# Kernel optimization log

Hardware: AMD Instinct MI355X
Metric: run time of the kernel (lower is better)

## Reference

```python
import jax, jax.numpy as jnp
import numpy as np

EPS = 1e-5
N, K, C = 32768, 27, 128


def setup_inputs() -> dict:
    key = jax.random.key(0)
    k1, k2, k3, k4 = jax.random.split(key, 4)
    feats = jax.random.normal(k1, (N, C), dtype=jnp.float32)
    # Precomputed kernel-offset neighbor map (MinkowskiEngine kernel map),
    # one input index per (point, kernel offset).
    neighbors = jax.random.randint(k2, (N, K), 0, N, dtype=jnp.int32)
    scale = 1.0 / np.sqrt(K * C)  # fan-in init like sparse conv
    W1 = jax.random.normal(k3, (K, C, C), dtype=jnp.float32) * scale
    W2 = jax.random.normal(k4, (K, C, C), dtype=jnp.float32) * scale
    g1 = jnp.ones((C,), jnp.float32)
    b1 = jnp.zeros((C,), jnp.float32)
    g2 = jnp.ones((C,), jnp.float32)
    b2 = jnp.zeros((C,), jnp.float32)
    return {"feats": feats, "neighbors": neighbors, "W1": W1, "g1": g1,
            "b1": b1, "W2": W2, "g2": g2, "b2": b2}


def _sparse_conv(f, nbr, W):
    # gather-GEMM-scatter: gather neighbor features per kernel offset,
    # contract with that offset's weight, sum over offsets.
    gathered = f[nbr]                      # [N, K, C]
    return jnp.einsum('nkc,kcd->nd', gathered, W)  # [N, C]


def _batch_norm(x, gamma, beta):
    mu = jnp.mean(x, axis=0)
    var = jnp.mean(jnp.square(x - mu), axis=0)
    return (x - mu) * jax.lax.rsqrt(var + EPS) * gamma + beta


def reference(feats, neighbors, W1, g1, b1, W2, g2, b2):
    out = _sparse_conv(feats, neighbors, W1)
    out = jax.nn.relu(_batch_norm(out, g1, b1))
    out = _sparse_conv(out, neighbors, W2)
    out = _batch_norm(out, g2, b2)
    return jax.nn.relu(out + feats)
```

## Files before the change

### kernel.cpp

```cpp
#include <hip/hip_runtime.h>
#include <stdint.h>

#define NPTS 32768
#define KOFF 27
#define CH   128
#define NC   (NPTS*CH)
#define KSPLIT 3
#define KPG  9
#define TILE_M 64
#define NITER (KPG*2)

typedef __attribute__((ext_vector_type(8))) short short8;
typedef __attribute__((ext_vector_type(4))) float f32x4;
typedef unsigned short u16;

__device__ __forceinline__ float bf2f(u16 u) {
    union { uint32_t i; float f; } v; v.i = ((uint32_t)u) << 16; return v.f;
}
__device__ __forceinline__ u16 f2bf(float f) {
    union { float f; uint32_t i; } v; v.f = f;
    return (u16)((v.i + 0x7FFF + ((v.i >> 16) & 1)) >> 16);
}

#define GLDS16(gp, lp) __builtin_amdgcn_global_load_lds( \
    (__attribute__((address_space(1))) void*)(gp),           \
    (__attribute__((address_space(3))) void*)(lp), 16, 0, 0)

__global__ __launch_bounds__(256)
void prep_kernel(const float* __restrict__ W1, const float* __restrict__ W2,
                 u16* __restrict__ W1t, u16* __restrict__ W2t,
                 const float* __restrict__ feats, u16* __restrict__ xbuf,
                 float* __restrict__ stat)
{
    __shared__ u16 t[128*129];
    const int b = blockIdx.x, tid = threadIdx.x;
    if (b < 2*KOFF) {
        if (b == 0) for (int i = tid; i < 512; i += 256) stat[i] = 0.0f;
        const float* src = (b < KOFF) ? W1 + (size_t)b*CH*CH : W2 + (size_t)(b-KOFF)*CH*CH;
        u16* dst         = (b < KOFF) ? W1t + (size_t)b*CH*CH : W2t + (size_t)(b-KOFF)*CH*CH;
        for (int e = tid; e < CH*CH; e += 256) {
            int c = e >> 7, d = e & 127;
            t[d*129 + c] = f2bf(src[e]);
        }
        __syncthreads();
        for (int e = tid; e < CH*CH; e += 256) {
            int d = e >> 7, c = e & 127;
            dst[e] = t[d*129 + c];
        }
    } else {
        size_t e = ((size_t)(b - 2*KOFF) * 256 + tid) * 8;
        float4 a = *(const float4*)(feats + e);
        float4 c = *(const float4*)(feats + e + 4);
        ushort4 lo, hi;
        lo.x = f2bf(a.x); lo.y = f2bf(a.y); lo.z = f2bf(a.z); lo.w = f2bf(a.w);
        hi.x = f2bf(c.x); hi.y = f2bf(c.y); hi.z = f2bf(c.z); hi.w = f2bf(c.w);
        *(ushort4*)(xbuf + e) = lo;
        *(ushort4*)(xbuf + e + 4) = hi;
    }
}

__global__ __launch_bounds__(256, 5)
void ResidualBlock_77498389889548_kernel(const u16* __restrict__ xb,
                                         const int* __restrict__ nbr,
                                         const u16* __restrict__ Wt,
                                         u16* __restrict__ part)
{
    __shared__ __align__(16) u16 A_lds[TILE_M*64];
    __shared__ __align__(16) u16 B_lds[CH*64];
    __shared__ int idx_lds[KPG*TILE_M];

    const int tid = threadIdx.x;
    const int n0  = blockIdx.x * TILE_M;
    const int kg  = blockIdx.y;

    for (int e = tid; e < KPG*TILE_M; e += 256) {
        int kk = e >> 6, r = e & 63;
        int nb = nbr[(size_t)(n0 + r)*KOFF + kg*KPG + kk];
        idx_lds[e] = ((unsigned)nb < (unsigned)NPTS) ? nb : 0;
    }
    __syncthreads();

    const int wave = tid >> 6;
    const int lane = tid & 63;
    const int wrow = (wave >> 1) * 32;
    const int wcol = (wave & 1) * 64;
    const int lm   = lane & 15;
    const int quad = lane >> 4;
    const int l8r  = lane >> 3;
    const int swz  = ((lane & 7) ^ l8r) << 3;

    f32x4 acc[2][4];
    #pragma unroll
    for (int i = 0; i < 2; ++i)
        #pragma unroll
        for (int j = 0; j < 4; ++j)
            #pragma unroll
            for (int r = 0; r < 4; ++r) acc[i][j][r] = 0.0f;

    int aoff[2][2], boff[2][4];
    #pragma unroll
    for (int kc = 0; kc < 2; ++kc) {
        int g = kc*4 + quad;
        #pragma unroll
        for (int i = 0; i < 2; ++i) {
            int row = wrow + i*16 + lm;
            aoff[kc][i] = row*128 + ((g ^ (row & 7)) << 4);
        }
        #pragma unroll
        for (int j = 0; j < 4; ++j) {
            int d = wcol + j*16 + lm;
            boff[kc][j] = d*128 + ((g ^ (d & 7)) << 4);
        }
    }

    const char* Ab = (const char*)A_lds;
    const char* Bb = (const char*)B_lds;

    for (int it = 0; it < NITER; ++it) {
        const int h  = (it >= KPG) ? 1 : 0;
        const int kk = it - h*KPG;

        #pragma unroll
        for (int j = 0; j < 2; ++j) {
            int row8 = wave*16 + j*8;
            int nb = idx_lds[kk*64 + row8 + l8r];
            GLDS16(xb + (size_t)nb*CH + h*64 + swz, &A_lds[row8*64]);
        }
        const u16* wb = Wt + (size_t)(kg*KPG + kk)*CH*CH + h*64 + swz;
        #pragma unroll
        for (int j = 0; j < 4; ++j) {
            int row8 = wave*32 + j*8;
            GLDS16(wb + (size_t)(row8 + l8r)*CH, &B_lds[row8*64]);
        }
        __syncthreads();

        #pragma unroll
        for (int kc = 0; kc < 2; ++kc) {
            short8 a[2], b[4];
            #pragma unroll
            for (int i = 0; i < 2; ++i) a[i] = *(const short8*)(Ab + aoff[kc][i]);
            #pragma unroll
            for (int j = 0; j < 4; ++j) b[j] = *(const short8*)(Bb + boff[kc][j]);
            #pragma unroll
            for (int i = 0; i < 2; ++i)
                #pragma unroll
                for (int j = 0; j < 4; ++j)
                    acc[i][j] = __builtin_amdgcn_mfma_f32_16x16x32_bf16(a[i], b[j], acc[i][j], 0, 0, 0);
        }
        __syncthreads();
    }

    u16* pb = part + (size_t)kg * NC;
    const int colb = wcol + lm;
    #pragma unroll
    for (int i = 0; i < 2; ++i) {
        #pragma unroll
        for (int r = 0; r < 4; ++r) {
            int row = n0 + wrow + i*16 + quad*4 + r;
            u16* pp = pb + (size_t)row*CH + colb;
            #pragma unroll
            for (int j = 0; j < 4; ++j) pp[j*16] = f2bf(acc[i][j][r]);
        }
    }
}

__global__ __launch_bounds__(256)
void sumstats_kernel(const u16* __restrict__ p0, const u16* __restrict__ p1,
                     const u16* __restrict__ p2, u16* __restrict__ y,
                     float* __restrict__ gsum, float* __restrict__ gsq)
{
    __shared__ float ls[CH], lq[CH];
    const int tid = threadIdx.x;
    const int c8 = (tid & 15) * 8;
    const int r0 = tid >> 4;
    const int b = blockIdx.x;
    if (tid < CH) { ls[tid] = 0.0f; lq[tid] = 0.0f; }
    __syncthreads();

    float s[8], q[8];
    #pragma unroll
    for (int i = 0; i < 8; ++i) { s[i] = 0.0f; q[i] = 0.0f; }

    for (int r = r0; r < 128; r += 16) {
        size_t e = (size_t)(b*128 + r)*CH + c8;
        ushort4 a0 = *(const ushort4*)(p0 + e), a1 = *(const ushort4*)(p0 + e + 4);
        ushort4 b0 = *(const ushort4*)(p1 + e), b1 = *(const ushort4*)(p1 + e + 4);
        ushort4 d0 = *(const ushort4*)(p2 + e), d1 = *(const ushort4*)(p2 + e + 4);
        float v[8];
        v[0] = bf2f(a0.x) + bf2f(b0.x) + bf2f(d0.x);
        v[1] = bf2f(a0.y) + bf2f(b0.y) + bf2f(d0.y);
        v[2] = bf2f(a0.z) + bf2f(b0.z) + bf2f(d0.z);
        v[3] = bf2f(a0.w) + bf2f(b0.w) + bf2f(d0.w);
        v[4] = bf2f(a1.x) + bf2f(b1.x) + bf2f(d1.x);
        v[5] = bf2f(a1.y) + bf2f(b1.y) + bf2f(d1.y);
        v[6] = bf2f(a1.z) + bf2f(b1.z) + bf2f(d1.z);
        v[7] = bf2f(a1.w) + bf2f(b1.w) + bf2f(d1.w);
        ushort4 o0, o1;
        o0.x = f2bf(v[0]); o0.y = f2bf(v[1]); o0.z = f2bf(v[2]); o0.w = f2bf(v[3]);
        o1.x = f2bf(v[4]); o1.y = f2bf(v[5]); o1.z = f2bf(v[6]); o1.w = f2bf(v[7]);
        *(ushort4*)(y + e) = o0;
        *(ushort4*)(y + e + 4) = o1;
        #pragma unroll
        for (int i = 0; i < 8; ++i) { s[i] += v[i]; q[i] += v[i]*v[i]; }
    }
    #pragma unroll
    for (int i = 0; i < 8; ++i) {
        atomicAdd(&ls[c8 + i], s[i]);
        atomicAdd(&lq[c8 + i], q[i]);
    }
    __syncthreads();
    if (tid < CH) {
        atomicAdd(&gsum[tid], ls[tid]);
        atomicAdd(&gsq[tid],  lq[tid]);
    }
}

__global__ __launch_bounds__(256)
void norm_relu_kernel(const u16* __restrict__ y, const float* __restrict__ sums,
                      const float* __restrict__ sumsq, const float* __restrict__ gam,
                      const float* __restrict__ bet, u16* __restrict__ xo)
{
    __shared__ float sc[128], sh[128];
    const int tid = threadIdx.x;
    if (tid < 128) {
        float mu  = sums[tid] * (1.0f/NPTS);
        float var = fmaxf(sumsq[tid] * (1.0f/NPTS) - mu*mu, 0.0f);
        float rs  = rsqrtf(var + 1e-5f);
        float s   = rs * gam[tid];
        sc[tid] = s; sh[tid] = bet[tid] - mu*s;
    }
    __syncthreads();
    size_t e = ((size_t)blockIdx.x*256 + tid) * 8;
    int c0 = (int)(e & 127);
    ushort4 lo = *(const ushort4*)(y + e);
    ushort4 hi = *(const ushort4*)(y + e + 4);
    ushort4 o0, o1;
    o0.x = f2bf(fmaxf(bf2f(lo.x)*sc[c0+0] + sh[c0+0], 0.0f));
    o0.y = f2bf(fmaxf(bf2f(lo.y)*sc[c0+1] + sh[c0+1], 0.0f));
    o0.z = f2bf(fmaxf(bf2f(lo.z)*sc[c0+2] + sh[c0+2], 0.0f));
    o0.w = f2bf(fmaxf(bf2f(lo.w)*sc[c0+3] + sh[c0+3], 0.0f));
    o1.x = f2bf(fmaxf(bf2f(hi.x)*sc[c0+4] + sh[c0+4], 0.0f));
    o1.y = f2bf(fmaxf(bf2f(hi.y)*sc[c0+5] + sh[c0+5], 0.0f));
    o1.z = f2bf(fmaxf(bf2f(hi.z)*sc[c0+6] + sh[c0+6], 0.0f));
    o1.w = f2bf(fmaxf(bf2f(hi.w)*sc[c0+7] + sh[c0+7], 0.0f));
    *(ushort4*)(xo + e) = o0;
    *(ushort4*)(xo + e + 4) = o1;
}

__global__ __launch_bounds__(256)
void final_kernel(const u16* __restrict__ y, const float* __restrict__ sums,
                  const float* __restrict__ sumsq, const float* __restrict__ gam,
                  const float* __restrict__ bet, const float* __restrict__ feats,
                  float* __restrict__ out)
{
    __shared__ float sc[128], sh[128];
    const int tid = threadIdx.x;
    if (tid < 128) {
        float mu  = sums[tid] * (1.0f/NPTS);
        float var = fmaxf(sumsq[tid] * (1.0f/NPTS) - mu*mu, 0.0f);
        float rs  = rsqrtf(var + 1e-5f);
        float s   = rs * gam[tid];
        sc[tid] = s; sh[tid] = bet[tid] - mu*s;
    }
    __syncthreads();
    size_t e = ((size_t)blockIdx.x*256 + tid) * 4;
    int c0 = (int)(e & 127);
    ushort4 in = *(const ushort4*)(y + e);
    float4 ft = *(const float4*)(feats + e);
    float4 o;
    o.x = fmaxf(bf2f(in.x)*sc[c0+0] + sh[c0+0] + ft.x, 0.0f);
    o.y = fmaxf(bf2f(in.y)*sc[c0+1] + sh[c0+1] + ft.y, 0.0f);
    o.z = fmaxf(bf2f(in.z)*sc[c0+2] + sh[c0+2] + ft.z, 0.0f);
    o.w = fmaxf(bf2f(in.w)*sc[c0+3] + sh[c0+3] + ft.w, 0.0f);
    *(float4*)(out + e) = o;
}

extern "C" void kernel_launch(void* const* d_in, const int* in_sizes, int n_in,
                              void* d_out, int out_size, void* d_ws, size_t ws_size,
                              hipStream_t stream)
{
    const float* feats = (const float*)d_in[0];
    const int*   nbr   = (const int*)d_in[1];
    const float* W1    = (const float*)d_in[2];
    const float* g1    = (const float*)d_in[3];
    const float* b1    = (const float*)d_in[4];
    const float* W2    = (const float*)d_in[5];
    const float* g2    = (const float*)d_in[6];
    const float* b2    = (const float*)d_in[7];
    float* out = (float*)d_out;

    char* ws = (char*)d_ws;
    u16*   xbuf = (u16*)ws;
    u16*   prt  = xbuf + (size_t)NC;
    u16*   ybuf = prt + (size_t)3*NC;
    u16*   W1t  = ybuf + (size_t)NC;
    u16*   W2t  = W1t + (size_t)KOFF*CH*CH;
    float* stat = (float*)(W2t + (size_t)KOFF*CH*CH);

    prep_kernel<<<dim3(2*KOFF + NC/2048), 256, 0, stream>>>(W1, W2, W1t, W2t, feats, xbuf, stat);

    ResidualBlock_77498389889548_kernel<<<dim3(NPTS/TILE_M, KSPLIT), 256, 0, stream>>>(
        xbuf, nbr, W1t, prt);
    sumstats_kernel<<<dim3(NPTS/128), 256, 0, stream>>>(
        prt, prt + (size_t)NC, prt + (size_t)2*NC, ybuf, stat, stat + 128);
    norm_relu_kernel<<<dim3(NC/2048), 256, 0, stream>>>(ybuf, stat, stat + 128, g1, b1, xbuf);

    ResidualBlock_77498389889548_kernel<<<dim3(NPTS/TILE_M, KSPLIT), 256, 0, stream>>>(
        xbuf, nbr, W2t, prt);
    sumstats_kernel<<<dim3(NPTS/128), 256, 0, stream>>>(
        prt, prt + (size_t)NC, prt + (size_t)2*NC, ybuf, stat + 256, stat + 384);
    final_kernel<<<dim3(NC/1024), 256, 0, stream>>>(ybuf, stat + 256, stat + 384, g2, b2, feats, out);
}
```

Before: 215.1 us.

## Fuse BN1 normalize+ReLU into second sparse-conv gather, drop norm_relu kernel

Removes the standalone norm_relu kernel. Its batch-norm scale/shift and ReLU now run inside a new conv2 kernel as it gathers neighbor rows from the un-normalized conv1 output. Each row is fetched with a register load, normalized, and written swizzled into LDS, instead of using the direct global-to-LDS path. This saves one full read and write pass over the feature map, but each gathered row is normalized once per use (27 times per point) and the gather goes through registers. The conv loop is also restructured into nested h/kk loops with the outer one unrolled, and sumstats now uses 64-row blocks for more parallelism.

```diff
diff --git a/kernel.cpp b/kernel.cpp
--- a/kernel.cpp
+++ b/kernel.cpp
@@ -8,7 +8,6 @@
 #define KSPLIT 3
 #define KPG  9
 #define TILE_M 64
-#define NITER (KPG*2)
 
 typedef __attribute__((ext_vector_type(8))) short short8;
 typedef __attribute__((ext_vector_type(4))) float f32x4;
@@ -116,38 +115,168 @@
     const char* Ab = (const char*)A_lds;
     const char* Bb = (const char*)B_lds;
 
-    for (int it = 0; it < NITER; ++it) {
-        const int h  = (it >= KPG) ? 1 : 0;
-        const int kk = it - h*KPG;
-
-        #pragma unroll
-        for (int j = 0; j < 2; ++j) {
-            int row8 = wave*16 + j*8;
-            int nb = idx_lds[kk*64 + row8 + l8r];
-            GLDS16(xb + (size_t)nb*CH + h*64 + swz, &A_lds[row8*64]);
-        }
-        const u16* wb = Wt + (size_t)(kg*KPG + kk)*CH*CH + h*64 + swz;
+    #pragma unroll
+    for (int h = 0; h < 2; ++h) {
+        for (int kk = 0; kk < KPG; ++kk) {
+            #pragma unroll
+            for (int j = 0; j < 2; ++j) {
+                int row8 = wave*16 + j*8;
+                int nb = idx_lds[kk*64 + row8 + l8r];
+                GLDS16(xb + (size_t)nb*CH + h*64 + swz, &A_lds[row8*64]);
+            }
+            const u16* wb = Wt + (size_t)(kg*KPG + kk)*CH*CH + h*64 + swz;
+            #pragma unroll
+            for (int j = 0; j < 4; ++j) {
+                int row8 = wave*32 + j*8;
+                GLDS16(wb + (size_t)(row8 + l8r)*CH, &B_lds[row8*64]);
+            }
+            __syncthreads();
+
+            #pragma unroll
+            for (int kc = 0; kc < 2; ++kc) {
+                short8 a[2], b[4];
+                #pragma unroll
+                for (int i = 0; i < 2; ++i) a[i] = *(const short8*)(Ab + aoff[kc][i]);
+                #pragma unroll
+                for (int j = 0; j < 4; ++j) b[j] = *(const short8*)(Bb + boff[kc][j]);
+                #pragma unroll
+                for (int i = 0; i < 2; ++i)
+                    #pragma unroll
+                    for (int j = 0; j < 4; ++j)
+                        acc[i][j] = __builtin_amdgcn_mfma_f32_16x16x32_bf16(a[i], b[j], acc[i][j], 0, 0, 0);
+            }
+            __syncthreads();
+        }
+    }
+
+    u16* pb = part + (size_t)kg * NC;
+    const int colb = wcol + lm;
+    #pragma unroll
+    for (int i = 0; i < 2; ++i) {
+        #pragma unroll
+        for (int r = 0; r < 4; ++r) {
+            int row = n0 + wrow + i*16 + quad*4 + r;
+            u16* pp = pb + (size_t)row*CH + colb;
+            #pragma unroll
+            for (int j = 0; j < 4; ++j) pp[j*16] = f2bf(acc[i][j][r]);
+        }
+    }
+}
+
+__global__ __launch_bounds__(256, 5)
+void conv2_kernel(const u16* __restrict__ yb,
+                  const int* __restrict__ nbr,
+                  const u16* __restrict__ Wt,
+                  const float* __restrict__ gsum, const float* __restrict__ gsq,
+                  const float* __restrict__ gam, const float* __restrict__ bet,
+                  u16* __restrict__ part)
+{
+    __shared__ __align__(16) u16 A_lds[TILE_M*64];
+    __shared__ __align__(16) u16 B_lds[CH*64];
+    __shared__ int idx_lds[KPG*TILE_M];
+    __shared__ float scs[CH], shs[CH];
+
+    const int tid = threadIdx.x;
+    const int n0  = blockIdx.x * TILE_M;
+    const int kg  = blockIdx.y;
+
+    if (tid < CH) {
+        float mu  = gsum[tid] * (1.0f/NPTS);
+        float var = fmaxf(gsq[tid] * (1.0f/NPTS) - mu*mu, 0.0f);
+        float rs  = rsqrtf(var + 1e-5f);
+        float s   = rs * gam[tid];
+        scs[tid] = s; shs[tid] = bet[tid] - mu*s;
+    }
+    for (int e = tid; e < KPG*TILE_M; e += 256) {
+        int kk = e >> 6, r = e & 63;
+        int nb = nbr[(size_t)(n0 + r)*KOFF + kg*KPG + kk];
+        idx_lds[e] = ((unsigned)nb < (unsigned)NPTS) ? nb : 0;
+    }
+    __syncthreads();
+
+    const int wave = tid >> 6;
+    const int lane = tid & 63;
+    const int wrow = (wave >> 1) * 32;
+    const int wcol = (wave & 1) * 64;
+    const int lm   = lane & 15;
+    const int quad = lane >> 4;
+    const int l8r  = lane >> 3;
+    const int swz  = ((lane & 7) ^ l8r) << 3;
+    const int srow = tid >> 3;
+    const int sci  = tid & 7;
+
+    f32x4 acc[2][4];
+    #pragma unroll
+    for (int i = 0; i < 2; ++i)
+        #pragma unroll
+        for (int j = 0; j < 4; ++j)
+            #pragma unroll
+            for (int r = 0; r < 4; ++r) acc[i][j][r] = 0.0f;
+
+    int aoff[2][2], boff[2][4];
+    #pragma unroll
+    for (int kc = 0; kc < 2; ++kc) {
+        int g = kc*4 + quad;
+        #pragma unroll
+        for (int i = 0; i < 2; ++i) {
+            int row = wrow + i*16 + lm;
+            aoff[kc][i] = row*128 + ((g ^ (row & 7)) << 4);
+        }
         #pragma unroll
         for (int j = 0; j < 4; ++j) {
-            int row8 = wave*32 + j*8;
-            GLDS16(wb + (size_t)(row8 + l8r)*CH, &B_lds[row8*64]);
-        }
-        __syncthreads();
-
-        #pragma unroll
-        for (int kc = 0; kc < 2; ++kc) {
-            short8 a[2], b[4];
-            #pragma unroll
-            for (int i = 0; i < 2; ++i) a[i] = *(const short8*)(Ab + aoff[kc][i]);
-            #pragma unroll
-            for (int j = 0; j < 4; ++j) b[j] = *(const short8*)(Bb + boff[kc][j]);
-            #pragma unroll
-            for (int i = 0; i < 2; ++i)
-                #pragma unroll
-                for (int j = 0; j < 4; ++j)
-                    acc[i][j] = __builtin_amdgcn_mfma_f32_16x16x32_bf16(a[i], b[j], acc[i][j], 0, 0, 0);
-        }
-        __syncthreads();
+            int d = wcol + j*16 + lm;
+            boff[kc][j] = d*128 + ((g ^ (d & 7)) << 4);
+        }
+    }
+
+    const char* Ab = (const char*)A_lds;
+    const char* Bb = (const char*)B_lds;
+
+    #pragma unroll
+    for (int h = 0; h < 2; ++h) {
+        float sc8[8], sh8[8];
+        #pragma unroll
+        for (int j = 0; j < 8; ++j) {
+            sc8[j] = scs[h*64 + sci*8 + j];
+            sh8[j] = shs[h*64 + sci*8 + j];
+        }
+        for (int kk = 0; kk < KPG; ++kk) {
+            #pragma unroll
+            for (int j = 0; j < 2; ++j) {
+                int row = j*32 + srow;
+                int nb  = idx_lds[kk*64 + row];
+                short8 v = *(const short8*)(yb + (size_t)nb*CH + h*64 + sci*8);
+                const u16* ve = (const u16*)&v;
+                short8 o;
+                u16* oe = (u16*)&o;
+                #pragma unroll
+                for (int t = 0; t < 8; ++t)
+                    oe[t] = f2bf(fmaxf(bf2f(ve[t])*sc8[t] + sh8[t], 0.0f));
+                *(short8*)((char*)A_lds + row*128 + ((sci ^ (row & 7)) << 4)) = o;
+            }
+            const u16* wb = Wt + (size_t)(kg*KPG + kk)*CH*CH + h*64 + swz;
+            #pragma unroll
+            for (int j = 0; j < 4; ++j) {
+                int row8 = wave*32 + j*8;
+                GLDS16(wb + (size_t)(row8 + l8r)*CH, &B_lds[row8*64]);
+            }
+            __syncthreads();
+
+            #pragma unroll
+            for (int kc = 0; kc < 2; ++kc) {
+                short8 a[2], b[4];
+                #pragma unroll
+                for (int i = 0; i < 2; ++i) a[i] = *(const short8*)(Ab + aoff[kc][i]);
+                #pragma unroll
+                for (int j = 0; j < 4; ++j) b[j] = *(const short8*)(Bb + boff[kc][j]);
+                #pragma unroll
+                for (int i = 0; i < 2; ++i)
+                    #pragma unroll
+                    for (int j = 0; j < 4; ++j)
+                        acc[i][j] = __builtin_amdgcn_mfma_f32_16x16x32_bf16(a[i], b[j], acc[i][j], 0, 0, 0);
+            }
+            __syncthreads();
+        }
     }
 
     u16* pb = part + (size_t)kg * NC;
@@ -181,8 +310,8 @@
     #pragma unroll
     for (int i = 0; i < 8; ++i) { s[i] = 0.0f; q[i] = 0.0f; }
 
-    for (int r = r0; r < 128; r += 16) {
-        size_t e = (size_t)(b*128 + r)*CH + c8;
+    for (int r = r0; r < 64; r += 16) {
+        size_t e = (size_t)(b*64 + r)*CH + c8;
         ushort4 a0 = *(const ushort4*)(p0 + e), a1 = *(const ushort4*)(p0 + e + 4);
         ushort4 b0 = *(const ushort4*)(p1 + e), b1 = *(const ushort4*)(p1 + e + 4);
         ushort4 d0 = *(const ushort4*)(p2 + e), d1 = *(const ushort4*)(p2 + e + 4);
@@ -216,38 +345,6 @@
 }
 
 __global__ __launch_bounds__(256)
-void norm_relu_kernel(const u16* __restrict__ y, const float* __restrict__ sums,
-                      const float* __restrict__ sumsq, const float* __restrict__ gam,
-                      const float* __restrict__ bet, u16* __restrict__ xo)
-{
-    __shared__ float sc[128], sh[128];
-    const int tid = threadIdx.x;
-    if (tid < 128) {
-        float mu  = sums[tid] * (1.0f/NPTS);
-        float var = fmaxf(sumsq[tid] * (1.0f/NPTS) - mu*mu, 0.0f);
-        float rs  = rsqrtf(var + 1e-5f);
-        float s   = rs * gam[tid];
-        sc[tid] = s; sh[tid] = bet[tid] - mu*s;
-    }
-    __syncthreads();
-    size_t e = ((size_t)blockIdx.x*256 + tid) * 8;
-    int c0 = (int)(e & 127);
-    ushort4 lo = *(const ushort4*)(y + e);
-    ushort4 hi = *(const ushort4*)(y + e + 4);
-    ushort4 o0, o1;
-    o0.x = f2bf(fmaxf(bf2f(lo.x)*sc[c0+0] + sh[c0+0], 0.0f));
-    o0.y = f2bf(fmaxf(bf2f(lo.y)*sc[c0+1] + sh[c0+1], 0.0f));
-    o0.z = f2bf(fmaxf(bf2f(lo.z)*sc[c0+2] + sh[c0+2], 0.0f));
-    o0.w = f2bf(fmaxf(bf2f(lo.w)*sc[c0+3] + sh[c0+3], 0.0f));
-    o1.x = f2bf(fmaxf(bf2f(hi.x)*sc[c0+4] + sh[c0+4], 0.0f));
-    o1.y = f2bf(fmaxf(bf2f(hi.y)*sc[c0+5] + sh[c0+5], 0.0f));
-    o1.z = f2bf(fmaxf(bf2f(hi.z)*sc[c0+6] + sh[c0+6], 0.0f));
-    o1.w = f2bf(fmaxf(bf2f(hi.w)*sc[c0+7] + sh[c0+7], 0.0f));
-    *(ushort4*)(xo + e) = o0;
-    *(ushort4*)(xo + e + 4) = o1;
-}
-
-__global__ __launch_bounds__(256)
 void final_kernel(const u16* __restrict__ y, const float* __restrict__ sums,
                   const float* __restrict__ sumsq, const float* __restrict__ gam,
                   const float* __restrict__ bet, const float* __restrict__ feats,
@@ -301,13 +398,12 @@
 
     ResidualBlock_77498389889548_kernel<<<dim3(NPTS/TILE_M, KSPLIT), 256, 0, stream>>>(
         xbuf, nbr, W1t, prt);
-    sumstats_kernel<<<dim3(NPTS/128), 256, 0, stream>>>(
+    sumstats_kernel<<<dim3(NPTS/64), 256, 0, stream>>>(
         prt, prt + (size_t)NC, prt + (size_t)2*NC, ybuf, stat, stat + 128);
-    norm_relu_kernel<<<dim3(NC/2048), 256, 0, stream>>>(ybuf, stat, stat + 128, g1, b1, xbuf);
-
-    ResidualBlock_77498389889548_kernel<<<dim3(NPTS/TILE_M, KSPLIT), 256, 0, stream>>>(
-        xbuf, nbr, W2t, prt);
-    sumstats_kernel<<<dim3(NPTS/128), 256, 0, stream>>>(
+
+    conv2_kernel<<<dim3(NPTS/TILE_M, KSPLIT), 256, 0, stream>>>(
+        ybuf, nbr, W2t, stat, stat + 128, g1, b1, prt);
+    sumstats_kernel<<<dim3(NPTS/64), 256, 0, stream>>>(
         prt, prt + (size_t)NC, prt + (size_t)2*NC, ybuf, stat + 256, stat + 384);
     final_kernel<<<dim3(NC/1024), 256, 0, stream>>>(ybuf, stat + 256, stat + 384, g2, b2, feats, out);
 }
```

Result: slower. 268.9 us (+25.0%).
